# Optimization experiments

Hardware: AMD Instinct MI355X
Metric: run time of the kernel (lower is better)

Reference implementation:

```python
import jax, jax.numpy as jnp
import numpy as np

T, N, E = 4, 4096, 65536
XD, HD, ZD = 256, 256, 64
EPS = 1e-10


def setup_inputs() -> dict:
    key = jax.random.key(0)
    ks = jax.random.split(key, 30)
    rn = lambda k, sh, s=0.05: jax.random.normal(k, sh, dtype=jnp.float32) * s
    inp = {
        "x": rn(ks[0], (T, N, XD), 1.0),
        "edge_idx": jax.random.randint(ks[1], (T, 2, E), 0, N, dtype=jnp.int32),
        "adj": jax.random.bernoulli(ks[2], 0.005, (T, N, N)).astype(jnp.float32),
        "eps_noise": jax.random.normal(ks[3], (T, N, ZD), dtype=jnp.float32),
        "h0": jnp.zeros((1, N, HD), jnp.float32),
        # phi_x / phi_z (Linear+ReLU)
        "phi_x_w": rn(ks[4], (XD, HD)), "phi_x_b": jnp.zeros((HD,), jnp.float32),
        "phi_z_w": rn(ks[5], (ZD, HD)), "phi_z_b": jnp.zeros((HD,), jnp.float32),
        # encoder GCNs
        "enc_w": rn(ks[6], (2 * HD, HD)), "enc_b": jnp.zeros((HD,), jnp.float32),
        "enc_mean_w": rn(ks[7], (HD, ZD)), "enc_mean_b": jnp.zeros((ZD,), jnp.float32),
        "enc_std_w": rn(ks[8], (HD, ZD)), "enc_std_b": jnp.zeros((ZD,), jnp.float32),
        # prior MLPs
        "prior_w": rn(ks[9], (HD, HD)), "prior_b": jnp.zeros((HD,), jnp.float32),
        "prior_mean_w": rn(ks[10], (HD, ZD)), "prior_mean_b": jnp.zeros((ZD,), jnp.float32),
        "prior_std_w": rn(ks[11], (HD, ZD)), "prior_std_b": jnp.zeros((ZD,), jnp.float32),
        # graph-GRU GCNs (bias=False, n_layers=1; x-input is cat[phi_x, phi_z] -> 2*HD)
        "gru_xz_w": rn(ks[12], (2 * HD, HD)), "gru_hz_w": rn(ks[13], (HD, HD)),
        "gru_xr_w": rn(ks[14], (2 * HD, HD)), "gru_hr_w": rn(ks[15], (HD, HD)),
        "gru_xh_w": rn(ks[16], (2 * HD, HD)), "gru_hh_w": rn(ks[17], (HD, HD)),
    }
    return inp


def _gcn(xf, src, dst, W, b):
    """GCNConv: sym-normalized (A + I) aggregation, then bias. Returns pre-activation."""
    h = xf @ W                                             # [N, out]
    deg = 1.0 + jax.ops.segment_sum(jnp.ones(src.shape[0], xf.dtype), dst, num_segments=N)
    dinv = jax.lax.rsqrt(deg)                              # [N]
    norm = dinv[src] * dinv[dst]                           # [E]
    agg = jax.ops.segment_sum(h[src] * norm[:, None], dst, num_segments=N)
    agg = agg + (dinv * dinv)[:, None] * h                 # self-loop term
    if b is not None:
        agg = agg + b
    return agg


def reference(x, edge_idx, adj, eps_noise, h0,
              phi_x_w, phi_x_b, phi_z_w, phi_z_b,
              enc_w, enc_b, enc_mean_w, enc_mean_b, enc_std_w, enc_std_b,
              prior_w, prior_b, prior_mean_w, prior_mean_b, prior_std_w, prior_std_b,
              gru_xz_w, gru_hz_w, gru_xr_w, gru_hr_w, gru_xh_w, gru_hh_w):
    relu, sp, sig = jax.nn.relu, jax.nn.softplus, jax.nn.sigmoid
    h = h0                                                  # [1, N, HD]
    kld = jnp.float32(0.0)
    nll = jnp.float32(0.0)
    enc_means, prior_means = [], []
    nn_f = jnp.float32(N * N)
    for t in range(T):
        src, dst = edge_idx[t, 0], edge_idx[t, 1]
        phi_x_t = relu(x[t] @ phi_x_w + phi_x_b)                       # [N, HD]
        enc_in = jnp.concatenate([phi_x_t, h[-1]], axis=1)             # [N, 2HD]
        enc_t = relu(_gcn(enc_in, src, dst, enc_w, enc_b))
        enc_mean_t = _gcn(enc_t, src, dst, enc_mean_w, enc_mean_b)     # act = identity
        enc_std_t = sp(_gcn(enc_t, src, dst, enc_std_w, enc_std_b))
        prior_t = relu(h[-1] @ prior_w + prior_b)
        prior_mean_t = prior_t @ prior_mean_w + prior_mean_b
        prior_std_t = sp(prior_t @ prior_std_w + prior_std_b)
        z_t = eps_noise[t] * enc_std_t + enc_mean_t                    # reparameterize
        phi_z_t = relu(z_t @ phi_z_w + phi_z_b)
        dec_t = sig(z_t @ z_t.T)                                       # [N, N] decode
        # graph-GRU step (n_layers = 1, bias=False)
        gin = jnp.concatenate([phi_x_t, phi_z_t], axis=1)              # [N, 2HD]
        z_g = sig(_gcn(gin, src, dst, gru_xz_w, None) + _gcn(h[0], src, dst, gru_hz_w, None))
        r_g = sig(_gcn(gin, src, dst, gru_xr_w, None) + _gcn(h[0], src, dst, gru_hr_w, None))
        h_tilde = jnp.tanh(_gcn(gin, src, dst, gru_xh_w, None)
                           + _gcn(r_g * h[0], src, dst, gru_hh_w, None))
        h = (z_g * h[0] + (1.0 - z_g) * h_tilde)[None]                 # [1, N, HD]
        # KLD (faithful to _kld_gauss, including its sign convention)
        s1, s2 = enc_std_t + EPS, prior_std_t + EPS
        kld_el = (2.0 * jnp.log(s2) - 2.0 * jnp.log(s1)
                  - (s1 * s1 + (enc_mean_t - prior_mean_t) ** 2) / (s2 * s2) + 1.0)
        kld = kld + (0.5 / N) * jnp.mean(jnp.sum(kld_el, axis=0))
        # NLL (faithful quirk: BCE-with-logits applied to sigmoid output dec_t)
        a = adj[t]
        tsum = jnp.sum(a)
        posw = (nn_f - tsum) / tsum
        norm = nn_f / ((nn_f - tsum) * 2.0)
        bce = posw * a * sp(-dec_t) + (1.0 - a) * sp(dec_t)
        nll = nll + norm * jnp.mean(bce)
        enc_means.append(enc_mean_t)
        prior_means.append(prior_mean_t)
    return kld, nll, jnp.stack(enc_means), jnp.stack(prior_means), h
```

## Files before the change

### kernel.cpp

```cpp
#include <hip/hip_runtime.h>
#include <hip/hip_bf16.h>

#define T_STEPS 4
#define N 4096
#define E 65536
#define XD 256
#define HD 256
#define ZD 64

typedef __hip_bfloat16 bf16;
typedef __attribute__((ext_vector_type(8))) short short8;
typedef __attribute__((ext_vector_type(4))) float f32x4;

__device__ __forceinline__ float b2f(bf16 v){ return __bfloat162float(v); }
__device__ __forceinline__ bf16 f2b(float v){ return __float2bfloat16(v); }
__device__ __forceinline__ short f2s(float v){ return __builtin_bit_cast(short, f2b(v)); }
__device__ __forceinline__ float bits2f(unsigned int s){ return __builtin_bit_cast(float, s << 16); }
__device__ __forceinline__ float s2f(short s){ return bits2f((unsigned int)(unsigned short)s); }
__device__ __forceinline__ float splus(float x){ return (x > 15.f) ? x : __logf(1.f + __expf(x)); }
__device__ __forceinline__ float sigm(float x){ return 1.f/(1.f + __expf(-x)); }
__device__ __forceinline__ float ftanh(float x){ return 2.f/(1.f + __expf(-2.f*x)) - 1.f; }

__device__ __forceinline__ float ldI(const void* p, size_t i, int f){
  return f ? ((const float*)p)[i] : b2f(((const bf16*)p)[i]);
}
__device__ __forceinline__ void stO(void* p, size_t i, float v, int f){
  if (f) ((float*)p)[i] = v; else ((bf16*)p)[i] = f2b(v);
}
__device__ __forceinline__ void ld8b(const bf16* p, float v[8]){
  uint4 u = *(const uint4*)p;
  v[0]=bits2f(u.x & 0xffffu); v[1]=bits2f(u.x >> 16);
  v[2]=bits2f(u.y & 0xffffu); v[3]=bits2f(u.y >> 16);
  v[4]=bits2f(u.z & 0xffffu); v[5]=bits2f(u.z >> 16);
  v[6]=bits2f(u.w & 0xffffu); v[7]=bits2f(u.w >> 16);
}
__device__ __forceinline__ void ldW8(const void* W, size_t off, int f, float w[8]){
  if (f == 0){ ld8b((const bf16*)W + off, w); }
  else {
    const float* Wf = (const float*)W + off;
    float4 a = *(const float4*)Wf, b = *(const float4*)(Wf + 4);
    w[0]=a.x; w[1]=a.y; w[2]=a.z; w[3]=a.w; w[4]=b.x; w[5]=b.y; w[6]=b.z; w[7]=b.w;
  }
}
__device__ __forceinline__ unsigned int pack2(float a, float b){
  return (unsigned int)(unsigned short)__builtin_bit_cast(unsigned short, f2b(a))
       | ((unsigned int)(unsigned short)__builtin_bit_cast(unsigned short, f2b(b)) << 16);
}
__device__ __forceinline__ uint4 pack8(const float v[8]){
  uint4 o; o.x = pack2(v[0],v[1]); o.y = pack2(v[2],v[3]);
  o.z = pack2(v[4],v[5]); o.w = pack2(v[6],v[7]);
  return o;
}

union SMem {
  struct { short As[64*40]; short Wt[64*40]; } g;
  struct { short Zi[64*72]; short Zj[64*72]; short Adj[64*72];
           float redA[256]; float redB[256]; float redC[256]; } z;
  struct { float msh[16*132]; } m;
  int sh[256];
  float red[256];
};

struct KP {
  const void *x, *adj, *eps, *h0;
  const int* ei;
  const void *phi_x_w, *phi_x_b, *phi_z_w, *phi_z_b;
  const void *enc_w, *enc_b, *enc_mean_w, *enc_mean_b, *enc_std_w, *enc_std_b;
  const void *prior_w, *prior_b, *prior_mean_w, *prior_mean_b, *prior_std_w, *prior_std_b;
  const void *gxz, *ghz, *gxr, *ghr, *gxh, *ghh;
  void* out;
  float* scal; int* dflag; float* dinv; int* offs; int* srcs; float* enorm; int* deg;
  float* h_prev; bf16* h_bf; bf16* phiXa; bf16* Tb1; bf16* Tb2;
  bf16* zbf; float* z_g; bf16* Gs1; bf16* Gsx; bf16* Gms; bf16* Gh2;
};

#define OUT_EM ((size_t)2)
#define OUT_PM ((size_t)(2 + (size_t)T_STEPS*N*ZD))
#define OUT_H  ((size_t)(2 + (size_t)2*T_STEPS*N*ZD))

__device__ void mfma_tile(SMem& sm, int tid, int f,
    const void* A1, int am1, int lda1, const void* A2, int am2, int lda2,
    int K1, int K, const void* W, int ldw, int wcol,
    const void* bias, int act, bf16* C, int ldc, int row0, int ccol0){
  int ar = tid >> 2, akk = (tid & 3)*8;
  int wk = tid >> 3, wn = (tid & 7)*8;
  int wave = tid >> 6, lane = tid & 63, m = lane & 15, kq = lane >> 4;
  f32x4 acc[4] = {};
  for (int k0 = 0; k0 < K; k0 += 32){
    const void* A; int am, lda, kb;
    if (k0 < K1){ A = A1; am = am1; lda = lda1; kb = k0; }
    else        { A = A2; am = am2; lda = lda2; kb = k0 - K1; }
    size_t aidx = (size_t)(row0 + ar)*lda + kb + akk;
    short8 av;
    if (am == 2 || (am == 1 && f == 0)){
      av = *(const short8*)((const short*)A + aidx);
    } else {
      const float* Af = (const float*)A;
      float4 u0 = *(const float4*)(Af + aidx);
      float4 u1 = *(const float4*)(Af + aidx + 4);
      av[0]=f2s(u0.x); av[1]=f2s(u0.y); av[2]=f2s(u0.z); av[3]=f2s(u0.w);
      av[4]=f2s(u1.x); av[5]=f2s(u1.y); av[6]=f2s(u1.z); av[7]=f2s(u1.w);
    }
    *(short8*)&sm.g.As[ar*40 + akk] = av;
    size_t wi = (size_t)(k0 + wk)*ldw + wcol + wn;
    float wf[8]; short wv[8];
    if (f == 0){
      short8 t8 = *(const short8*)((const short*)W + wi);
      #pragma unroll
      for (int j = 0; j < 8; j++) wv[j] = t8[j];
    } else {
      ldW8(W, wi, f, wf);
      #pragma unroll
      for (int j = 0; j < 8; j++) wv[j] = f2s(wf[j]);
    }
    #pragma unroll
    for (int j = 0; j < 8; j++){
      int nrow = wn + j;
      int col = (((wk >> 3) ^ ((nrow >> 3) & 3)) << 3) | (wk & 7);
      sm.g.Wt[nrow*40 + col] = wv[j];
    }
    __syncthreads();
    short8 afr = *(const short8*)&sm.g.As[(wave*16 + m)*40 + kq*8];
    #pragma unroll
    for (int t4 = 0; t4 < 4; t4++){
      int nb = t4*16 + m;
      short8 bfr = *(const short8*)&sm.g.Wt[nb*40 + ((kq ^ ((nb >> 3) & 3)) << 3)];
      acc[t4] = __builtin_amdgcn_mfma_f32_16x16x32_bf16(afr, bfr, acc[t4], 0, 0, 0);
    }
    __syncthreads();
  }
  #pragma unroll
  for (int t4 = 0; t4 < 4; t4++){
    int c = ccol0 + t4*16 + m;
    float bv = bias ? ldI(bias, wcol + t4*16 + m, f) : 0.f;
    #pragma unroll
    for (int reg = 0; reg < 4; reg++){
      int r = row0 + wave*16 + kq*4 + reg;
      float v = acc[t4][reg] + bv;
      if (act == 1) v = fmaxf(v, 0.f);
      C[(size_t)r*ldc + c] = f2b(v);
    }
  }
}

__device__ void dec_tile1(const KP& p, SMem& sm, int tid, int t, int u, int f){
  int i0 = (u >> 6)*64, j0 = (u & 63)*64;
  size_t aoff = (size_t)t*N*N;
  #pragma unroll
  for (int i = 0; i < 2; i++){
    int idx = tid + i*256;
    int r = idx >> 3, c = idx & 7;
    int col = ((c ^ ((r >> 3) & 3)) << 3);
    *(short8*)&sm.z.Zi[r*72 + col] = *(const short8*)((const short*)p.zbf + (size_t)(i0+r)*ZD + c*8);
    *(short8*)&sm.z.Zj[r*72 + col] = *(const short8*)((const short*)p.zbf + (size_t)(j0+r)*ZD + c*8);
  }
  {
    int row = tid >> 2, c0 = (tid & 3)*16;
    if (f){
      const float* ap = (const float*)p.adj + aoff + (size_t)(i0+row)*N + j0 + c0;
      short tmp[16];
      #pragma unroll
      for (int q = 0; q < 16; q += 4){
        float4 v = *(const float4*)(ap + q);
        tmp[q]=f2s(v.x); tmp[q+1]=f2s(v.y); tmp[q+2]=f2s(v.z); tmp[q+3]=f2s(v.w);
      }
      *(short8*)&sm.z.Adj[row*72 + c0]     = *(short8*)&tmp[0];
      *(short8*)&sm.z.Adj[row*72 + c0 + 8] = *(short8*)&tmp[8];
    } else {
      const short* ap = (const short*)p.adj + aoff + (size_t)(i0+row)*N + j0 + c0;
      *(short8*)&sm.z.Adj[row*72 + c0]     = *(const short8*)ap;
      *(short8*)&sm.z.Adj[row*72 + c0 + 8] = *(const short8*)(ap + 8);
    }
  }
  __syncthreads();
  int wave = tid >> 6, lane = tid & 63, m = lane & 15, kq = lane >> 4;
  int ra = wave*16 + m, sa = (ra >> 3) & 3;
  short8 a1 = *(const short8*)&sm.z.Zi[ra*72 + ((kq ^ sa) << 3)];
  short8 a2 = *(const short8*)&sm.z.Zi[ra*72 + (((kq+4) ^ sa) << 3)];
  f32x4 acc[4] = {};
  #pragma unroll
  for (int t4 = 0; t4 < 4; t4++){
    int rb = t4*16 + m, sb2 = (rb >> 3) & 3;
    short8 b1 = *(const short8*)&sm.z.Zj[rb*72 + ((kq ^ sb2) << 3)];
    short8 b2 = *(const short8*)&sm.z.Zj[rb*72 + (((kq+4) ^ sb2) << 3)];
    acc[t4] = __builtin_amdgcn_mfma_f32_16x16x32_bf16(a1, b1, acc[t4], 0, 0, 0);
    acc[t4] = __builtin_amdgcn_mfma_f32_16x16x32_bf16(a2, b2, acc[t4], 0, 0, 0);
  }
  float lts = 0.f, lP = 0.f, lQ = 0.f;
  #pragma unroll
  for (int t4 = 0; t4 < 4; t4++){
    int lj = t4*16 + m;
    #pragma unroll
    for (int reg = 0; reg < 4; reg++){
      int li = wave*16 + kq*4 + reg;
      float av = s2f(sm.z.Adj[li*72 + lj]);
      float dec = sigm(acc[t4][reg]);
      lts += av;
      lQ += (1.f - av)*splus(dec);
      if (av != 0.f) lP += av*splus(-dec);
    }
  }
  __syncthreads();
  sm.z.redA[tid] = lts; sm.z.redB[tid] = lP; sm.z.redC[tid] = lQ;
  __syncthreads();
  for (int o = 128; o > 0; o >>= 1){
    if (tid < o){
      sm.z.redA[tid] += sm.z.redA[tid+o];
      sm.z.redB[tid] += sm.z.redB[tid+o];
      sm.z.redC[tid] += sm.z.redC[tid+o];
    }
    __syncthreads();
  }
  if (tid == 0){
    atomicAdd(p.scal + 8 + t,  sm.z.redA[0]);
    atomicAdd(p.scal + 12 + t, sm.z.redB[0]);
    atomicAdd(p.scal + 16 + t, sm.z.redC[0]);
  }
}

__global__ __launch_bounds__(256) void setup0_k(KP p){
  int gb = blockIdx.x, tid = threadIdx.x;
  if (gb == 0){ if (tid < 64) p.scal[tid] = 0.f; }
  else if (gb == 1){
    if (tid == 0){
      const unsigned short* u = (const unsigned short*)p.x;
      int big = 0;
      for (int i = 0; i < 256; i++){ int e = (u[i] >> 7) & 0xFF; if (e >= 134) big++; }
      *p.dflag = (big > 16) ? 1 : 0;
    }
  } else {
    p.deg[(gb-2)*256 + tid] = 0;
  }
}

__global__ __launch_bounds__(256) void count_deg_k(KP p){
  int idx = blockIdx.x*256 + threadIdx.x;
  int t = idx >> 16, e = idx & (E-1);
  int dst = p.ei[(size_t)t*2*E + E + e] & (N-1);
  atomicAdd(&p.deg[t*N + dst], 1);
}

__global__ __launch_bounds__(256) void setup2_k(KP p){
  __shared__ SMem sm;
  int gb = blockIdx.x, tid = threadIdx.x;
  int f = *p.dflag;
  if (gb < 4){
    int t = gb;
    const int* dg = p.deg + t*N;
    int* of = p.offs + t*(N+1);
    int base = tid*16;
    int loc[16]; int s = 0;
    #pragma unroll
    for (int i = 0; i < 16; i++){ loc[i] = s; s += dg[base+i]; }
    sm.sh[tid] = s;
    __syncthreads();
    for (int o = 1; o < 256; o <<= 1){
      int v = (tid >= o) ? sm.sh[tid-o] : 0;
      __syncthreads();
      sm.sh[tid] += v;
      __syncthreads();
    }
    int pre = (tid == 0) ? 0 : sm.sh[tid-1];
    #pragma unroll
    for (int i = 0; i < 16; i++){
      int deg_i = dg[base+i];
      of[base+i] = pre + loc[i];
      p.dinv[t*N + base + i] = rsqrtf(1.f + (float)deg_i);
    }
    if (tid == 255) of[N] = sm.sh[255];
    __syncthreads();
    #pragma unroll
    for (int i = 0; i < 16; i++) p.deg[t*N + base + i] = pre + loc[i];
  } else if (gb < 36){
    for (int idx = (gb-4)*256 + tid; idx < N*HD; idx += 32*256){
      float v = ldI(p.h0, idx, f);
      p.h_prev[idx] = v; p.h_bf[idx] = f2b(v);
    }
  } else {
    int u = gb - 36;
    int colblk = u & 3, rowblk = u >> 2;
    mfma_tile(sm, tid, f, p.x, 1, XD, nullptr, 0, 0, XD, XD,
              p.phi_x_w, HD, colblk*64, p.phi_x_b, 1,
              p.phiXa, HD, rowblk*64, colblk*64);
  }
}

__global__ __launch_bounds__(256) void g1_k(KP p, int t){
  __shared__ SMem sm;
  int gb = blockIdx.x, tid = threadIdx.x, f = *p.dflag;
  if (gb >= 1024){
    int idx = (gb - 1024)*256 + tid;
    int tt = idx >> 16, e = idx & (E-1);
    int s = p.ei[(size_t)tt*2*E + e] & (N-1);
    int d = p.ei[(size_t)tt*2*E + E + e] & (N-1);
    int pos = atomicAdd(&p.deg[tt*N + d], 1);
    if (pos >= 0 && pos < E){
      p.srcs[(size_t)tt*E + pos] = s;
      p.enorm[(size_t)tt*E + pos] = p.dinv[tt*N + s] * p.dinv[tt*N + d];
    }
    return;
  }
  const bf16* phiX = p.phiXa + (size_t)t*N*HD;
  int colblk = gb & 15, rowblk = gb >> 4;
  int grp = colblk >> 2, c4 = colblk & 3;
  if (grp == 0)
    mfma_tile(sm, tid, f, phiX, 2, HD, p.h_bf, 2, HD, 256, 512,
              p.enc_w, HD, c4*64, nullptr, 0, p.Gs1, 1024, rowblk*64, colblk*64);
  else if (grp == 1)
    mfma_tile(sm, tid, f, p.h_bf, 2, HD, nullptr, 0, 0, 256, 256,
              p.prior_w, HD, c4*64, p.prior_b, 1, p.Gs1, 1024, rowblk*64, colblk*64);
  else if (grp == 2)
    mfma_tile(sm, tid, f, p.h_bf, 2, HD, nullptr, 0, 0, 256, 256,
              p.ghz, HD, c4*64, nullptr, 0, p.Gs1, 1024, rowblk*64, colblk*64);
  else
    mfma_tile(sm, tid, f, p.h_bf, 2, HD, nullptr, 0, 0, 256, 256,
              p.ghr, HD, c4*64, nullptr, 0, p.Gs1, 1024, rowblk*64, colblk*64);
}

__global__ __launch_bounds__(256) void encagg_pms_k(KP p, int t){
  __shared__ SMem sm;
  int gb = blockIdx.x, tid = threadIdx.x, f = *p.dflag;
  const int* offs_t = p.offs + t*(N+1);
  const int* srcs_t = p.srcs + (size_t)t*E;
  const float* en_t = p.enorm + (size_t)t*E;
  const float* dv_t = p.dinv + t*N;
  if (gb < 512){
    int g8 = tid >> 5, l = tid & 31;
    int n = gb*8 + g8, c = l*8;
    int e0 = offs_t[n], e1 = offs_t[n+1];
    float d2 = dv_t[n]*dv_t[n];
    float acc[8], va[8], vb[8];
    ld8b(p.Gs1 + (size_t)n*1024 + c, va);
    #pragma unroll
    for (int j = 0; j < 8; j++) acc[j] = d2 * va[j];
    int e = e0;
    for (; e + 1 < e1; e += 2){
      int s0 = srcs_t[e] & (N-1), s1 = srcs_t[e+1] & (N-1);
      float n0 = en_t[e], n1 = en_t[e+1];
      ld8b(p.Gs1 + (size_t)s0*1024 + c, va);
      ld8b(p.Gs1 + (size_t)s1*1024 + c, vb);
      #pragma unroll
      for (int j = 0; j < 8; j++) acc[j] += n0*va[j] + n1*vb[j];
    }
    if (e < e1){
      int s0 = srcs_t[e] & (N-1);
      float n0 = en_t[e];
      ld8b(p.Gs1 + (size_t)s0*1024 + c, va);
      #pragma unroll
      for (int j = 0; j < 8; j++) acc[j] += n0*va[j];
    }
    #pragma unroll
    for (int j = 0; j < 8; j++) acc[j] = fmaxf(acc[j] + ldI(p.enc_b, c + j, f), 0.f);
    *(uint4*)(p.Tb1 + (size_t)n*HD + c) = pack8(acc);
  } else {
    int u = gb - 512;
    int colblk = u & 1, rowblk = u >> 1;
    mfma_tile(sm, tid, f, p.Gs1 + 256, 2, 1024, nullptr, 0, 0, 256, 256,
              colblk ? p.prior_std_w : p.prior_mean_w, ZD, 0,
              colblk ? p.prior_std_b : p.prior_mean_b, 0,
              p.Gms, 256, rowblk*64, 128 + colblk*64);
  }
}

__global__ __launch_bounds__(256) void encms_k(KP p, int t){
  __shared__ SMem sm;
  int gb = blockIdx.x, tid = threadIdx.x, f = *p.dflag;
  int colblk = gb & 1, rowblk = gb >> 1;
  mfma_tile(sm, tid, f, p.Tb1, 2, HD, nullptr, 0, 0, 256, 256,
            colblk ? p.enc_std_w : p.enc_mean_w, ZD, 0, nullptr, 0,
            p.Gms, 256, rowblk*64, colblk*64);
}

__global__ __launch_bounds__(256) void msaggpost_k(KP p, int t){
  __shared__ SMem sm;
  int gb = blockIdx.x, tid = threadIdx.x, f = *p.dflag;
  const int* offs_t = p.offs + t*(N+1);
  const int* srcs_t = p.srcs + (size_t)t*E;
  const float* en_t = p.enorm + (size_t)t*E;
  const float* dv_t = p.dinv + t*N;
  int g16 = tid >> 4, l = tid & 15;
  int n = gb*16 + g16, c = l*8;
  {
    int e0 = offs_t[n], e1 = offs_t[n+1];
    float d2 = dv_t[n]*dv_t[n];
    float acc[8], va[8], vb[8];
    ld8b(p.Gms + (size_t)n*256 + c, va);
    #pragma unroll
    for (int j = 0; j < 8; j++) acc[j] = d2 * va[j];
    int e = e0;
    for (; e + 1 < e1; e += 2){
      int s0 = srcs_t[e] & (N-1), s1 = srcs_t[e+1] & (N-1);
      float n0 = en_t[e], n1 = en_t[e+1];
      ld8b(p.Gms + (size_t)s0*256 + c, va);
      ld8b(p.Gms + (size_t)s1*256 + c, vb);
      #pragma unroll
      for (int j = 0; j < 8; j++) acc[j] += n0*va[j] + n1*vb[j];
    }
    if (e < e1){
      int s0 = srcs_t[e] & (N-1);
      float n0 = en_t[e];
      ld8b(p.Gms + (size_t)s0*256 + c, va);
      #pragma unroll
      for (int j = 0; j < 8; j++) acc[j] += n0*va[j];
    }
    #pragma unroll
    for (int j = 0; j < 8; j++) sm.m.msh[g16*132 + c + j] = acc[j];
  }
  __syncthreads();
  float el = 0.f;
  {
    int d0 = l*4;
    #pragma unroll
    for (int q = 0; q < 4; q++){
      int d = d0 + q;
      size_t idx = (size_t)n*ZD + d;
      float mean = sm.m.msh[g16*132 + d] + ldI(p.enc_mean_b, d, f);
      float sd = splus(sm.m.msh[g16*132 + 64 + d] + ldI(p.enc_std_b, d, f));
      float zv = ldI(p.eps, (size_t)t*N*ZD + idx, f)*sd + mean;
      p.zbf[idx] = f2b(zv);
      stO(p.out, OUT_EM + (size_t)t*N*ZD + idx, mean, f);
      float pm = b2f(p.Gms[(size_t)n*256 + 128 + d]);
      float ps = splus(b2f(p.Gms[(size_t)n*256 + 192 + d]));
      stO(p.out, OUT_PM + (size_t)t*N*ZD + idx, pm, f);
      float s1 = sd + 1e-10f, s2 = ps + 1e-10f;
      float dm = mean - pm;
      el += 2.f*(__logf(s2) - __logf(s1)) - (s1*s1 + dm*dm)/(s2*s2) + 1.f;
    }
  }
  __syncthreads();
  sm.red[tid] = el; __syncthreads();
  for (int o = 128; o > 0; o >>= 1){ if (tid < o) sm.red[tid] += sm.red[tid+o]; __syncthreads(); }
  if (tid == 0) atomicAdd(p.scal + 4, sm.red[0] * (0.5f/((float)N*(float)ZD)));
}

__global__ __launch_bounds__(256) void phiz_k(KP p, int t){
  __shared__ SMem sm;
  int gb = blockIdx.x, tid = threadIdx.x, f = *p.dflag;
  int colblk = gb & 3, rowblk = gb >> 2;
  mfma_tile(sm, tid, f, p.zbf, 2, ZD, nullptr, 0, 0, ZD, ZD,
            p.phi_z_w, HD, colblk*64, p.phi_z_b, 1, p.Tb2, HD, rowblk*64, colblk*64);
}

__global__ __launch_bounds__(256) void grux_dec_k(KP p, int t){
  __shared__ SMem sm;
  int gb = blockIdx.x, tid = threadIdx.x, f = *p.dflag;
  if (gb < 768){
    const bf16* phiX = p.phiXa + (size_t)t*N*HD;
    int colblk = gb % 12, rowblk = gb / 12;
    int grp = colblk >> 2, c4 = colblk & 3;
    const void* W = (grp == 0) ? p.gxz : ((grp == 1) ? p.gxr : p.gxh);
    mfma_tile(sm, tid, f, phiX, 2, HD, p.Tb2, 2, HD, 256, 512,
              W, HD, c4*64, nullptr, 0, p.Gsx, 768, rowblk*64, colblk*64);
  } else {
    dec_tile1(p, sm, tid, t, gb - 768, f);
  }
}

__global__ __launch_bounds__(256) void zr_k(KP p, int t){
  int gb = blockIdx.x, tid = threadIdx.x;
  const int* offs_t = p.offs + t*(N+1);
  const int* srcs_t = p.srcs + (size_t)t*E;
  const float* en_t = p.enorm + (size_t)t*E;
  const float* dv_t = p.dinv + t*N;
  int g4 = tid >> 6, lane = tid & 63;
  int n = gb*4 + g4, c = lane*8;
  int e0 = offs_t[n], e1 = offs_t[n+1];
  float d2 = dv_t[n]*dv_t[n];
  float acc[8], v1[8], v2[8], v3[8], v4[8];
  ld8b(p.Gsx + (size_t)n*768 + c, v1);
  ld8b(p.Gs1 + 512 + (size_t)n*1024 + c, v2);
  #pragma unroll
  for (int j = 0; j < 8; j++) acc[j] = d2 * (v1[j] + v2[j]);
  int e = e0;
  for (; e + 1 < e1; e += 2){
    int s0 = srcs_t[e] & (N-1), s1 = srcs_t[e+1] & (N-1);
    float n0 = en_t[e], n1 = en_t[e+1];
    ld8b(p.Gsx + (size_t)s0*768 + c, v1);
    ld8b(p.Gs1 + 512 + (size_t)s0*1024 + c, v2);
    ld8b(p.Gsx + (size_t)s1*768 + c, v3);
    ld8b(p.Gs1 + 512 + (size_t)s1*1024 + c, v4);
    #pragma unroll
    for (int j = 0; j < 8; j++) acc[j] += n0*(v1[j] + v2[j]) + n1*(v3[j] + v4[j]);
  }
  if (e < e1){
    int s0 = srcs_t[e] & (N-1);
    float n0 = en_t[e];
    ld8b(p.Gsx + (size_t)s0*768 + c, v1);
    ld8b(p.Gs1 + 512 + (size_t)s0*1024 + c, v2);
    #pragma unroll
    for (int j = 0; j < 8; j++) acc[j] += n0*(v1[j] + v2[j]);
  }
  if (c < 256){
    size_t base = (size_t)n*HD + c;
    float4 o0, o1;
    o0.x = sigm(acc[0]); o0.y = sigm(acc[1]); o0.z = sigm(acc[2]); o0.w = sigm(acc[3]);
    o1.x = sigm(acc[4]); o1.y = sigm(acc[5]); o1.z = sigm(acc[6]); o1.w = sigm(acc[7]);
    *(float4*)(p.z_g + base) = o0;
    *(float4*)(p.z_g + base + 4) = o1;
  } else {
    size_t base = (size_t)n*HD + (c - 256);
    float r[8];
    #pragma unroll
    for (int j = 0; j < 8; j++) r[j] = sigm(acc[j]) * p.h_prev[base+j];
    *(uint4*)(p.Tb1 + base) = pack8(r);
  }
}

__global__ __launch_bounds__(256) void hh_k(KP p, int t){
  __shared__ SMem sm;
  int gb = blockIdx.x, tid = threadIdx.x, f = *p.dflag;
  int colblk = gb & 3, rowblk = gb >> 2;
  mfma_tile(sm, tid, f, p.Tb1, 2, HD, nullptr, 0, 0, 256, 256,
            p.ghh, HD, colblk*64, nullptr, 0, p.Gh2, 256, rowblk*64, colblk*64);
}

__global__ __launch_bounds__(256) void hagg_k(KP p, int t){
  int gb = blockIdx.x, tid = threadIdx.x, f = *p.dflag;
  if (gb >= 512){
    if (tid == 0){
      const float NNf = 16777216.f;
      float nll = 0.f;
      for (int tt = 0; tt < T_STEPS; tt++){
        float ts = p.scal[8+tt], P = p.scal[12+tt], Q = p.scal[16+tt];
        float posw = (NNf - ts)/ts;
        nll += (posw*P + Q) * 0.5f/(NNf - ts);
      }
      stO(p.out, 0, p.scal[4], f);
      stO(p.out, 1, nll, f);
    }
    return;
  }
  const int* offs_t = p.offs + t*(N+1);
  const int* srcs_t = p.srcs + (size_t)t*E;
  const float* en_t = p.enorm + (size_t)t*E;
  const float* dv_t = p.dinv + t*N;
  int g8 = tid >> 5, l = tid & 31;
  int n = gb*8 + g8, c = l*8;
  int e0 = offs_t[n], e1 = offs_t[n+1];
  float d2 = dv_t[n]*dv_t[n];
  float acc[8], v1[8], v2[8], v3[8], v4[8];
  ld8b(p.Gsx + 512 + (size_t)n*768 + c, v1);
  ld8b(p.Gh2 + (size_t)n*256 + c, v2);
  #pragma unroll
  for (int j = 0; j < 8; j++) acc[j] = d2 * (v1[j] + v2[j]);
  int e = e0;
  for (; e + 1 < e1; e += 2){
    int s0 = srcs_t[e] & (N-1), s1 = srcs_t[e+1] & (N-1);
    float n0 = en_t[e], n1 = en_t[e+1];
    ld8b(p.Gsx + 512 + (size_t)s0*768 + c, v1);
    ld8b(p.Gh2 + (size_t)s0*256 + c, v2);
    ld8b(p.Gsx + 512 + (size_t)s1*768 + c, v3);
    ld8b(p.Gh2 + (size_t)s1*256 + c, v4);
    #pragma unroll
    for (int j = 0; j < 8; j++) acc[j] += n0*(v1[j] + v2[j]) + n1*(v3[j] + v4[j]);
  }
  if (e < e1){
    int s0 = srcs_t[e] & (N-1);
    float n0 = en_t[e];
    ld8b(p.Gsx + 512 + (size_t)s0*768 + c, v1);
    ld8b(p.Gh2 + (size_t)s0*256 + c, v2);
    #pragma unroll
    for (int j = 0; j < 8; j++) acc[j] += n0*(v1[j] + v2[j]);
  }
  size_t base = (size_t)n*HD + c;
  #pragma unroll
  for (int j = 0; j < 8; j++){
    float z = p.z_g[base+j];
    float hv = p.h_prev[base+j];
    float nv = z*hv + (1.f - z)*ftanh(acc[j]);
    p.h_prev[base+j] = nv;
    p.h_bf[base+j] = f2b(nv);
    if (t == T_STEPS-1) stO(p.out, OUT_H + base + j, nv, f);
  }
}

extern "C" void kernel_launch(void* const* d_in, const int* in_sizes, int n_in,
                              void* d_out, int out_size, void* d_ws, size_t ws_size,
                              hipStream_t stream){
  KP P;
  P.x = d_in[0];  P.ei = (const int*)d_in[1];  P.adj = d_in[2];  P.eps = d_in[3];  P.h0 = d_in[4];
  P.phi_x_w = d_in[5];  P.phi_x_b = d_in[6];  P.phi_z_w = d_in[7];  P.phi_z_b = d_in[8];
  P.enc_w = d_in[9];  P.enc_b = d_in[10];
  P.enc_mean_w = d_in[11];  P.enc_mean_b = d_in[12];
  P.enc_std_w = d_in[13];   P.enc_std_b = d_in[14];
  P.prior_w = d_in[15];  P.prior_b = d_in[16];
  P.prior_mean_w = d_in[17];  P.prior_mean_b = d_in[18];
  P.prior_std_w = d_in[19];   P.prior_std_b = d_in[20];
  P.gxz = d_in[21];  P.ghz = d_in[22];  P.gxr = d_in[23];
  P.ghr = d_in[24];  P.gxh = d_in[25];  P.ghh = d_in[26];
  P.out = d_out;

  char* wp = (char*)d_ws;
  auto alloc = [&](size_t bytes){ void* q = (void*)wp; wp += (bytes + 255) & ~(size_t)255; return q; };
  P.scal  = (float*)alloc(64*sizeof(float));
  P.dflag = (int*)  alloc(256);
  P.dinv  = (float*)alloc((size_t)T_STEPS*N*4);
  P.offs  = (int*)  alloc((size_t)T_STEPS*(N+1)*4);
  P.srcs  = (int*)  alloc((size_t)T_STEPS*E*4);
  P.enorm = (float*)alloc((size_t)T_STEPS*E*4);
  P.deg   = (int*)  alloc((size_t)T_STEPS*N*4);
  P.h_prev= (float*)alloc((size_t)N*HD*4);
  P.h_bf  = (bf16*) alloc((size_t)N*HD*2);
  P.phiXa = (bf16*) alloc((size_t)T_STEPS*N*HD*2);
  P.Tb1   = (bf16*) alloc((size_t)N*HD*2);
  P.Tb2   = (bf16*) alloc((size_t)N*HD*2);
  P.zbf   = (bf16*) alloc((size_t)N*ZD*2);
  P.z_g   = (float*)alloc((size_t)N*HD*4);
  P.Gs1   = (bf16*) alloc((size_t)N*1024*2);
  P.Gsx   = (bf16*) alloc((size_t)N*768*2);
  P.Gms   = (bf16*) alloc((size_t)N*256*2);
  P.Gh2   = (bf16*) alloc((size_t)N*256*2);

  setup0_k<<<66,256,0,stream>>>(P);
  count_deg_k<<<1024,256,0,stream>>>(P);
  setup2_k<<<1060,256,0,stream>>>(P);
  for (int t = 0; t < T_STEPS; t++){
    g1_k<<<(t == 0) ? 2048 : 1024,256,0,stream>>>(P, t);
    encagg_pms_k<<<640,256,0,stream>>>(P, t);
    encms_k<<<128,256,0,stream>>>(P, t);
    msaggpost_k<<<256,256,0,stream>>>(P, t);
    phiz_k<<<256,256,0,stream>>>(P, t);
    grux_dec_k<<<4864,256,0,stream>>>(P, t);
    zr_k<<<1024,256,0,stream>>>(P, t);
    hh_k<<<256,256,0,stream>>>(P, t);
    hagg_k<<<(t == T_STEPS-1) ? 513 : 512,256,0,stream>>>(P, t);
  }
}
```

Baseline: 1.401 ms.

## Precompute phi_x GEMMs for all steps, fuse encoder aggregation with mean/std GEMM

All phi_x-dependent products (encoder and the three GRU x-gates) are computed up front for every timestep in a new batched setup kernel. Per-step GEMMs now cover only the h or phi_z half of K and add the precomputed half in the epilogue. The generic MFMA tile now processes 64-wide K chunks per sync. The encoder aggregation and the enc mean/std projection are merged into one kernel that keeps the aggregated rows in LDS, removing a launch and a round trip through memory. This costs an extra 32 MB buffer and larger shared-memory tiles, which may lower occupancy.

```diff
diff --git a/kernel.cpp b/kernel.cpp
--- a/kernel.cpp
+++ b/kernel.cpp
@@ -51,15 +51,17 @@
   o.z = pack2(v[4],v[5]); o.w = pack2(v[6],v[7]);
   return o;
 }
-
-union SMem {
-  struct { short As[64*40]; short Wt[64*40]; } g;
-  struct { short Zi[64*72]; short Zj[64*72]; short Adj[64*72];
-           float redA[256]; float redB[256]; float redC[256]; } z;
-  struct { float msh[16*132]; } m;
-  int sh[256];
-  float red[256];
-};
+__device__ __forceinline__ unsigned int pack2s(short a, short b){
+  return (unsigned int)(unsigned short)a | ((unsigned int)(unsigned short)b << 16);
+}
+__device__ __forceinline__ const void* wofs(const void* W, int f, size_t elems){
+  return f ? (const void*)((const float*)W + elems) : (const void*)((const bf16*)W + elems);
+}
+
+struct GemmSM { short As[64*72]; short Wt[64*72]; };
+struct DecSM  { short Zi[64*72]; short Zj[64*72]; short Adj[64*72];
+                float redA[256]; float redB[256]; float redC[256]; };
+struct EncSM  { short At[16*264]; short Wt[128*40]; };
 
 struct KP {
   const void *x, *adj, *eps, *h0;
@@ -72,60 +74,70 @@
   float* scal; int* dflag; float* dinv; int* offs; int* srcs; float* enorm; int* deg;
   float* h_prev; bf16* h_bf; bf16* phiXa; bf16* Tb1; bf16* Tb2;
   bf16* zbf; float* z_g; bf16* Gs1; bf16* Gsx; bf16* Gms; bf16* Gh2;
+  bf16* PreB;
 };
 
 #define OUT_EM ((size_t)2)
 #define OUT_PM ((size_t)(2 + (size_t)T_STEPS*N*ZD))
 #define OUT_H  ((size_t)(2 + (size_t)2*T_STEPS*N*ZD))
 
-__device__ void mfma_tile(SMem& sm, int tid, int f,
-    const void* A1, int am1, int lda1, const void* A2, int am2, int lda2,
-    int K1, int K, const void* W, int ldw, int wcol,
-    const void* bias, int act, bf16* C, int ldc, int row0, int ccol0){
-  int ar = tid >> 2, akk = (tid & 3)*8;
-  int wk = tid >> 3, wn = (tid & 7)*8;
+__device__ void mfma_tile(GemmSM& sm, int tid, int f,
+    const void* A, int am, int lda, int K,
+    const void* W, int ldw, int wcol,
+    const void* bias, int act, bf16* C, int ldc, int row0, int ccol0,
+    const bf16* pre, int ldpre){
+  int ar = tid >> 2, akk = (tid & 3)*16;
+  int kp2 = (tid >> 3)*2, wn = (tid & 7)*8;
   int wave = tid >> 6, lane = tid & 63, m = lane & 15, kq = lane >> 4;
   f32x4 acc[4] = {};
-  for (int k0 = 0; k0 < K; k0 += 32){
-    const void* A; int am, lda, kb;
-    if (k0 < K1){ A = A1; am = am1; lda = lda1; kb = k0; }
-    else        { A = A2; am = am2; lda = lda2; kb = k0 - K1; }
-    size_t aidx = (size_t)(row0 + ar)*lda + kb + akk;
-    short8 av;
-    if (am == 2 || (am == 1 && f == 0)){
-      av = *(const short8*)((const short*)A + aidx);
+  for (int k0 = 0; k0 < K; k0 += 64){
+    size_t aidx = (size_t)(row0 + ar)*lda + k0 + akk;
+    short8 av0, av1;
+    if (am == 2 || f == 0){
+      av0 = *(const short8*)((const short*)A + aidx);
+      av1 = *(const short8*)((const short*)A + aidx + 8);
     } else {
-      const float* Af = (const float*)A;
-      float4 u0 = *(const float4*)(Af + aidx);
-      float4 u1 = *(const float4*)(Af + aidx + 4);
-      av[0]=f2s(u0.x); av[1]=f2s(u0.y); av[2]=f2s(u0.z); av[3]=f2s(u0.w);
-      av[4]=f2s(u1.x); av[5]=f2s(u1.y); av[6]=f2s(u1.z); av[7]=f2s(u1.w);
-    }
-    *(short8*)&sm.g.As[ar*40 + akk] = av;
-    size_t wi = (size_t)(k0 + wk)*ldw + wcol + wn;
-    float wf[8]; short wv[8];
+      const float* Af = (const float*)A + aidx;
+      float4 u0 = *(const float4*)(Af);
+      float4 u1 = *(const float4*)(Af + 4);
+      float4 u2 = *(const float4*)(Af + 8);
+      float4 u3 = *(const float4*)(Af + 12);
+      av0[0]=f2s(u0.x); av0[1]=f2s(u0.y); av0[2]=f2s(u0.z); av0[3]=f2s(u0.w);
+      av0[4]=f2s(u1.x); av0[5]=f2s(u1.y); av0[6]=f2s(u1.z); av0[7]=f2s(u1.w);
+      av1[0]=f2s(u2.x); av1[1]=f2s(u2.y); av1[2]=f2s(u2.z); av1[3]=f2s(u2.w);
+      av1[4]=f2s(u3.x); av1[5]=f2s(u3.y); av1[6]=f2s(u3.z); av1[7]=f2s(u3.w);
+    }
+    size_t wi = (size_t)(k0 + kp2)*ldw + wcol + wn;
+    short w0[8], w1[8];
     if (f == 0){
-      short8 t8 = *(const short8*)((const short*)W + wi);
-      #pragma unroll
-      for (int j = 0; j < 8; j++) wv[j] = t8[j];
+      short8 t0 = *(const short8*)((const short*)W + wi);
+      short8 t1 = *(const short8*)((const short*)W + wi + ldw);
+      #pragma unroll
+      for (int j = 0; j < 8; j++){ w0[j] = t0[j]; w1[j] = t1[j]; }
     } else {
-      ldW8(W, wi, f, wf);
-      #pragma unroll
-      for (int j = 0; j < 8; j++) wv[j] = f2s(wf[j]);
-    }
+      float wf0[8], wf1[8];
+      ldW8(W, wi, 1, wf0); ldW8(W, wi + ldw, 1, wf1);
+      #pragma unroll
+      for (int j = 0; j < 8; j++){ w0[j] = f2s(wf0[j]); w1[j] = f2s(wf1[j]); }
+    }
+    *(short8*)&sm.As[ar*72 + akk]     = av0;
+    *(short8*)&sm.As[ar*72 + akk + 8] = av1;
     #pragma unroll
     for (int j = 0; j < 8; j++){
       int nrow = wn + j;
-      int col = (((wk >> 3) ^ ((nrow >> 3) & 3)) << 3) | (wk & 7);
-      sm.g.Wt[nrow*40 + col] = wv[j];
+      int col = (((kp2 >> 3) ^ ((nrow >> 3) & 7)) << 3) | (kp2 & 7);
+      *(unsigned int*)&sm.Wt[nrow*72 + col] = pack2s(w0[j], w1[j]);
     }
     __syncthreads();
-    short8 afr = *(const short8*)&sm.g.As[(wave*16 + m)*40 + kq*8];
+    short8 afr0 = *(const short8*)&sm.As[(wave*16 + m)*72 + kq*8];
+    short8 afr1 = *(const short8*)&sm.As[(wave*16 + m)*72 + (kq + 4)*8];
     #pragma unroll
     for (int t4 = 0; t4 < 4; t4++){
-      int nb = t4*16 + m;
-      short8 bfr = *(const short8*)&sm.g.Wt[nb*40 + ((kq ^ ((nb >> 3) & 3)) << 3)];
-      acc[t4] = __builtin_amdgcn_mfma_f32_16x16x32_bf16(afr, bfr, acc[t4], 0, 0, 0);
+      int nb = t4*16 + m, sb = (nb >> 3) & 7;
+      short8 b0 = *(const short8*)&sm.Wt[nb*72 + ((kq ^ sb) << 3)];
+      short8 b1 = *(const short8*)&sm.Wt[nb*72 + (((kq + 4) ^ sb) << 3)];
+      acc[t4] = __builtin_amdgcn_mfma_f32_16x16x32_bf16(afr0, b0, acc[t4], 0, 0, 0);
+      acc[t4] = __builtin_amdgcn_mfma_f32_16x16x32_bf16(afr1, b1, acc[t4], 0, 0, 0);
     }
     __syncthreads();
   }
@@ -137,13 +149,14 @@
     for (int reg = 0; reg < 4; reg++){
       int r = row0 + wave*16 + kq*4 + reg;
       float v = acc[t4][reg] + bv;
+      if (pre) v += b2f(pre[(size_t)r*ldpre + t4*16 + m]);
       if (act == 1) v = fmaxf(v, 0.f);
       C[(size_t)r*ldc + c] = f2b(v);
     }
   }
 }
 
-__device__ void dec_tile1(const KP& p, SMem& sm, int tid, int t, int u, int f){
+__device__ void dec_tile1(const KP& p, DecSM& d, int tid, int t, int u, int f){
   int i0 = (u >> 6)*64, j0 = (u & 63)*64;
   size_t aoff = (size_t)t*N*N;
   #pragma unroll
@@ -151,8 +164,8 @@
     int idx = tid + i*256;
     int r = idx >> 3, c = idx & 7;
     int col = ((c ^ ((r >> 3) & 3)) << 3);
-    *(short8*)&sm.z.Zi[r*72 + col] = *(const short8*)((const short*)p.zbf + (size_t)(i0+r)*ZD + c*8);
-    *(short8*)&sm.z.Zj[r*72 + col] = *(const short8*)((const short*)p.zbf + (size_t)(j0+r)*ZD + c*8);
+    *(short8*)&d.Zi[r*72 + col] = *(const short8*)((const short*)p.zbf + (size_t)(i0+r)*ZD + c*8);
+    *(short8*)&d.Zj[r*72 + col] = *(const short8*)((const short*)p.zbf + (size_t)(j0+r)*ZD + c*8);
   }
   {
     int row = tid >> 2, c0 = (tid & 3)*16;
@@ -164,25 +177,25 @@
         float4 v = *(const float4*)(ap + q);
         tmp[q]=f2s(v.x); tmp[q+1]=f2s(v.y); tmp[q+2]=f2s(v.z); tmp[q+3]=f2s(v.w);
       }
-      *(short8*)&sm.z.Adj[row*72 + c0]     = *(short8*)&tmp[0];
-      *(short8*)&sm.z.Adj[row*72 + c0 + 8] = *(short8*)&tmp[8];
+      *(short8*)&d.Adj[row*72 + c0]     = *(short8*)&tmp[0];
+      *(short8*)&d.Adj[row*72 + c0 + 8] = *(short8*)&tmp[8];
     } else {
       const short* ap = (const short*)p.adj + aoff + (size_t)(i0+row)*N + j0 + c0;
-      *(short8*)&sm.z.Adj[row*72 + c0]     = *(const short8*)ap;
-      *(short8*)&sm.z.Adj[row*72 + c0 + 8] = *(const short8*)(ap + 8);
+      *(short8*)&d.Adj[row*72 + c0]     = *(const short8*)ap;
+      *(short8*)&d.Adj[row*72 + c0 + 8] = *(const short8*)(ap + 8);
     }
   }
   __syncthreads();
   int wave = tid >> 6, lane = tid & 63, m = lane & 15, kq = lane >> 4;
   int ra = wave*16 + m, sa = (ra >> 3) & 3;
-  short8 a1 = *(const short8*)&sm.z.Zi[ra*72 + ((kq ^ sa) << 3)];
-  short8 a2 = *(const short8*)&sm.z.Zi[ra*72 + (((kq+4) ^ sa) << 3)];
+  short8 a1 = *(const short8*)&d.Zi[ra*72 + ((kq ^ sa) << 3)];
+  short8 a2 = *(const short8*)&d.Zi[ra*72 + (((kq+4) ^ sa) << 3)];
   f32x4 acc[4] = {};
   #pragma unroll
   for (int t4 = 0; t4 < 4; t4++){
     int rb = t4*16 + m, sb2 = (rb >> 3) & 3;
-    short8 b1 = *(const short8*)&sm.z.Zj[rb*72 + ((kq ^ sb2) << 3)];
-    short8 b2 = *(const short8*)&sm.z.Zj[rb*72 + (((kq+4) ^ sb2) << 3)];
+    short8 b1 = *(const short8*)&d.Zj[rb*72 + ((kq ^ sb2) << 3)];
+    short8 b2 = *(const short8*)&d.Zj[rb*72 + (((kq+4) ^ sb2) << 3)];
     acc[t4] = __builtin_amdgcn_mfma_f32_16x16x32_bf16(a1, b1, acc[t4], 0, 0, 0);
     acc[t4] = __builtin_amdgcn_mfma_f32_16x16x32_bf16(a2, b2, acc[t4], 0, 0, 0);
   }
@@ -193,7 +206,7 @@
     #pragma unroll
     for (int reg = 0; reg < 4; reg++){
       int li = wave*16 + kq*4 + reg;
-      float av = s2f(sm.z.Adj[li*72 + lj]);
+      float av = s2f(d.Adj[li*72 + lj]);
       float dec = sigm(acc[t4][reg]);
       lts += av;
       lQ += (1.f - av)*splus(dec);
@@ -201,20 +214,20 @@
     }
   }
   __syncthreads();
-  sm.z.redA[tid] = lts; sm.z.redB[tid] = lP; sm.z.redC[tid] = lQ;
+  d.redA[tid] = lts; d.redB[tid] = lP; d.redC[tid] = lQ;
   __syncthreads();
   for (int o = 128; o > 0; o >>= 1){
     if (tid < o){
-      sm.z.redA[tid] += sm.z.redA[tid+o];
-      sm.z.redB[tid] += sm.z.redB[tid+o];
-      sm.z.redC[tid] += sm.z.redC[tid+o];
+      d.redA[tid] += d.redA[tid+o];
+      d.redB[tid] += d.redB[tid+o];
+      d.redC[tid] += d.redC[tid+o];
     }
     __syncthreads();
   }
   if (tid == 0){
-    atomicAdd(p.scal + 8 + t,  sm.z.redA[0]);
-    atomicAdd(p.scal + 12 + t, sm.z.redB[0]);
-    atomicAdd(p.scal + 16 + t, sm.z.redC[0]);
+    atomicAdd(p.scal + 8 + t,  d.redA[0]);
+    atomicAdd(p.scal + 12 + t, d.redB[0]);
+    atomicAdd(p.scal + 16 + t, d.redC[0]);
   }
 }
 
@@ -241,7 +254,7 @@
 }
 
 __global__ __launch_bounds__(256) void setup2_k(KP p){
-  __shared__ SMem sm;
+  __shared__ union { int sh[256]; GemmSM g; } sm;
   int gb = blockIdx.x, tid = threadIdx.x;
   int f = *p.dflag;
   if (gb < 4){
@@ -279,14 +292,29 @@
   } else {
     int u = gb - 36;
     int colblk = u & 3, rowblk = u >> 2;
-    mfma_tile(sm, tid, f, p.x, 1, XD, nullptr, 0, 0, XD, XD,
+    mfma_tile(sm.g, tid, f, p.x, 1, XD, XD,
               p.phi_x_w, HD, colblk*64, p.phi_x_b, 1,
-              p.phiXa, HD, rowblk*64, colblk*64);
-  }
+              p.phiXa, HD, rowblk*64, colblk*64, nullptr, 0);
+  }
+}
+
+__global__ __launch_bounds__(256) void setup3_k(KP p){
+  __shared__ GemmSM sm;
+  int gb = blockIdx.x, tid = threadIdx.x, f = *p.dflag;
+  int colblk = gb & 15, rowblk = gb >> 4;
+  int grp = colblk >> 2, c4 = colblk & 3;
+  const void* W;
+  if (grp == 0) W = p.enc_w;
+  else if (grp == 1) W = p.gxz;
+  else if (grp == 2) W = p.gxr;
+  else W = p.gxh;
+  mfma_tile(sm, tid, f, p.phiXa, 2, HD, 256,
+            W, HD, c4*64, nullptr, 0,
+            p.PreB, 1024, rowblk*64, colblk*64, nullptr, 0);
 }
 
 __global__ __launch_bounds__(256) void g1_k(KP p, int t){
-  __shared__ SMem sm;
+  __shared__ GemmSM sm;
   int gb = blockIdx.x, tid = threadIdx.x, f = *p.dflag;
   if (gb >= 1024){
     int idx = (gb - 1024)*256 + tid;
@@ -300,79 +328,126 @@
     }
     return;
   }
-  const bf16* phiX = p.phiXa + (size_t)t*N*HD;
+  const bf16* preT = p.PreB + (size_t)t*N*1024;
   int colblk = gb & 15, rowblk = gb >> 4;
   int grp = colblk >> 2, c4 = colblk & 3;
   if (grp == 0)
-    mfma_tile(sm, tid, f, phiX, 2, HD, p.h_bf, 2, HD, 256, 512,
-              p.enc_w, HD, c4*64, nullptr, 0, p.Gs1, 1024, rowblk*64, colblk*64);
+    mfma_tile(sm, tid, f, p.h_bf, 2, HD, 256,
+              wofs(p.enc_w, f, (size_t)256*HD), HD, c4*64, nullptr, 0,
+              p.Gs1, 1024, rowblk*64, colblk*64, preT + c4*64, 1024);
   else if (grp == 1)
-    mfma_tile(sm, tid, f, p.h_bf, 2, HD, nullptr, 0, 0, 256, 256,
-              p.prior_w, HD, c4*64, p.prior_b, 1, p.Gs1, 1024, rowblk*64, colblk*64);
+    mfma_tile(sm, tid, f, p.h_bf, 2, HD, 256,
+              p.prior_w, HD, c4*64, p.prior_b, 1,
+              p.Gs1, 1024, rowblk*64, colblk*64, nullptr, 0);
   else if (grp == 2)
-    mfma_tile(sm, tid, f, p.h_bf, 2, HD, nullptr, 0, 0, 256, 256,
-              p.ghz, HD, c4*64, nullptr, 0, p.Gs1, 1024, rowblk*64, colblk*64);
+    mfma_tile(sm, tid, f, p.h_bf, 2, HD, 256,
+              p.ghz, HD, c4*64, nullptr, 0,
+              p.Gs1, 1024, rowblk*64, colblk*64, nullptr, 0);
   else
-    mfma_tile(sm, tid, f, p.h_bf, 2, HD, nullptr, 0, 0, 256, 256,
-              p.ghr, HD, c4*64, nullptr, 0, p.Gs1, 1024, rowblk*64, colblk*64);
-}
-
-__global__ __launch_bounds__(256) void encagg_pms_k(KP p, int t){
-  __shared__ SMem sm;
+    mfma_tile(sm, tid, f, p.h_bf, 2, HD, 256,
+              p.ghr, HD, c4*64, nullptr, 0,
+              p.Gs1, 1024, rowblk*64, colblk*64, nullptr, 0);
+}
+
+__global__ __launch_bounds__(256) void encfused_k(KP p, int t){
+  __shared__ union { EncSM e; GemmSM g; } sm;
   int gb = blockIdx.x, tid = threadIdx.x, f = *p.dflag;
+  if (gb >= 256){
+    int u = gb - 256;
+    int colblk = u & 1, rowblk = u >> 1;
+    mfma_tile(sm.g, tid, f, p.Gs1 + 256, 2, 1024, 256,
+              colblk ? p.prior_std_w : p.prior_mean_w, ZD, 0,
+              colblk ? p.prior_std_b : p.prior_mean_b, 0,
+              p.Gms, 256, rowblk*64, 128 + colblk*64, nullptr, 0);
+    return;
+  }
   const int* offs_t = p.offs + t*(N+1);
   const int* srcs_t = p.srcs + (size_t)t*E;
   const float* en_t = p.enorm + (size_t)t*E;
   const float* dv_t = p.dinv + t*N;
-  if (gb < 512){
-    int g8 = tid >> 5, l = tid & 31;
-    int n = gb*8 + g8, c = l*8;
+  int g16 = tid >> 4, l = tid & 15;
+  int n = gb*16 + g16, c = l*16;
+  {
     int e0 = offs_t[n], e1 = offs_t[n+1];
     float d2 = dv_t[n]*dv_t[n];
-    float acc[8], va[8], vb[8];
+    float acc[16], va[8], vb[8], vc[8], vd[8];
     ld8b(p.Gs1 + (size_t)n*1024 + c, va);
-    #pragma unroll
-    for (int j = 0; j < 8; j++) acc[j] = d2 * va[j];
+    ld8b(p.Gs1 + (size_t)n*1024 + c + 8, vb);
+    #pragma unroll
+    for (int j = 0; j < 8; j++){ acc[j] = d2*va[j]; acc[8+j] = d2*vb[j]; }
     int e = e0;
     for (; e + 1 < e1; e += 2){
       int s0 = srcs_t[e] & (N-1), s1 = srcs_t[e+1] & (N-1);
       float n0 = en_t[e], n1 = en_t[e+1];
       ld8b(p.Gs1 + (size_t)s0*1024 + c, va);
-      ld8b(p.Gs1 + (size_t)s1*1024 + c, vb);
-      #pragma unroll
-      for (int j = 0; j < 8; j++) acc[j] += n0*va[j] + n1*vb[j];
+      ld8b(p.Gs1 + (size_t)s0*1024 + c + 8, vb);
+      ld8b(p.Gs1 + (size_t)s1*1024 + c, vc);
+      ld8b(p.Gs1 + (size_t)s1*1024 + c + 8, vd);
+      #pragma unroll
+      for (int j = 0; j < 8; j++){ acc[j] += n0*va[j] + n1*vc[j]; acc[8+j] += n0*vb[j] + n1*vd[j]; }
     }
     if (e < e1){
       int s0 = srcs_t[e] & (N-1);
       float n0 = en_t[e];
       ld8b(p.Gs1 + (size_t)s0*1024 + c, va);
-      #pragma unroll
-      for (int j = 0; j < 8; j++) acc[j] += n0*va[j];
-    }
-    #pragma unroll
-    for (int j = 0; j < 8; j++) acc[j] = fmaxf(acc[j] + ldI(p.enc_b, c + j, f), 0.f);
-    *(uint4*)(p.Tb1 + (size_t)n*HD + c) = pack8(acc);
-  } else {
-    int u = gb - 512;
-    int colblk = u & 1, rowblk = u >> 1;
-    mfma_tile(sm, tid, f, p.Gs1 + 256, 2, 1024, nullptr, 0, 0, 256, 256,
-              colblk ? p.prior_std_w : p.prior_mean_w, ZD, 0,
-              colblk ? p.prior_std_b : p.prior_mean_b, 0,
-              p.Gms, 256, rowblk*64, 128 + colblk*64);
-  }
-}
-
-__global__ __launch_bounds__(256) void encms_k(KP p, int t){
-  __shared__ SMem sm;
-  int gb = blockIdx.x, tid = threadIdx.x, f = *p.dflag;
-  int colblk = gb & 1, rowblk = gb >> 1;
-  mfma_tile(sm, tid, f, p.Tb1, 2, HD, nullptr, 0, 0, 256, 256,
-            colblk ? p.enc_std_w : p.enc_mean_w, ZD, 0, nullptr, 0,
-            p.Gms, 256, rowblk*64, colblk*64);
+      ld8b(p.Gs1 + (size_t)s0*1024 + c + 8, vb);
+      #pragma unroll
+      for (int j = 0; j < 8; j++){ acc[j] += n0*va[j]; acc[8+j] += n0*vb[j]; }
+    }
+    #pragma unroll
+    for (int j = 0; j < 16; j++) acc[j] = fmaxf(acc[j] + ldI(p.enc_b, c + j, f), 0.f);
+    *(uint4*)&sm.e.At[g16*264 + c]     = pack8(acc);
+    *(uint4*)&sm.e.At[g16*264 + c + 8] = pack8(acc + 8);
+  }
+  int wave = tid >> 6, lane = tid & 63, m = lane & 15, kq = lane >> 4;
+  int kp2e = (tid >> 4)*2;
+  int wn2 = (tid & 15)*8;
+  f32x4 acc2[2] = {};
+  for (int k0 = 0; k0 < 256; k0 += 32){
+    const void* Wp = (wn2 < 64) ? p.enc_mean_w : p.enc_std_w;
+    int wc = wn2 & 63;
+    size_t wi = (size_t)(k0 + kp2e)*ZD + wc;
+    short w0[8], w1[8];
+    if (f == 0){
+      short8 t0 = *(const short8*)((const short*)Wp + wi);
+      short8 t1 = *(const short8*)((const short*)Wp + wi + ZD);
+      #pragma unroll
+      for (int j = 0; j < 8; j++){ w0[j] = t0[j]; w1[j] = t1[j]; }
+    } else {
+      float wf0[8], wf1[8];
+      ldW8(Wp, wi, 1, wf0); ldW8(Wp, wi + ZD, 1, wf1);
+      #pragma unroll
+      for (int j = 0; j < 8; j++){ w0[j] = f2s(wf0[j]); w1[j] = f2s(wf1[j]); }
+    }
+    #pragma unroll
+    for (int j = 0; j < 8; j++){
+      int nrow = wn2 + j;
+      int col = (((kp2e >> 3) ^ ((nrow >> 3) & 3)) << 3) | (kp2e & 7);
+      *(unsigned int*)&sm.e.Wt[nrow*40 + col] = pack2s(w0[j], w1[j]);
+    }
+    __syncthreads();
+    short8 afr = *(const short8*)&sm.e.At[m*264 + k0 + kq*8];
+    #pragma unroll
+    for (int t2 = 0; t2 < 2; t2++){
+      int nb = wave*32 + t2*16 + m, sb = (nb >> 3) & 3;
+      short8 bfr = *(const short8*)&sm.e.Wt[nb*40 + ((kq ^ sb) << 3)];
+      acc2[t2] = __builtin_amdgcn_mfma_f32_16x16x32_bf16(afr, bfr, acc2[t2], 0, 0, 0);
+    }
+    __syncthreads();
+  }
+  #pragma unroll
+  for (int t2 = 0; t2 < 2; t2++){
+    int cc = wave*32 + t2*16 + m;
+    #pragma unroll
+    for (int reg = 0; reg < 4; reg++){
+      int node = gb*16 + kq*4 + reg;
+      p.Gms[(size_t)node*256 + cc] = f2b(acc2[t2][reg]);
+    }
+  }
 }
 
 __global__ __launch_bounds__(256) void msaggpost_k(KP p, int t){
-  __shared__ SMem sm;
+  __shared__ union { float msh[16*132]; float red[256]; } sm;
   int gb = blockIdx.x, tid = threadIdx.x, f = *p.dflag;
   const int* offs_t = p.offs + t*(N+1);
   const int* srcs_t = p.srcs + (size_t)t*E;
@@ -404,7 +479,7 @@
       for (int j = 0; j < 8; j++) acc[j] += n0*va[j];
     }
     #pragma unroll
-    for (int j = 0; j < 8; j++) sm.m.msh[g16*132 + c + j] = acc[j];
+    for (int j = 0; j < 8; j++) sm.msh[g16*132 + c + j] = acc[j];
   }
   __syncthreads();
   float el = 0.f;
@@ -414,8 +489,8 @@
     for (int q = 0; q < 4; q++){
       int d = d0 + q;
       size_t idx = (size_t)n*ZD + d;
-      float mean = sm.m.msh[g16*132 + d] + ldI(p.enc_mean_b, d, f);
-      float sd = splus(sm.m.msh[g16*132 + 64 + d] + ldI(p.enc_std_b, d, f));
+      float mean = sm.msh[g16*132 + d] + ldI(p.enc_mean_b, d, f);
+      float sd = splus(sm.msh[g16*132 + 64 + d] + ldI(p.enc_std_b, d, f));
       float zv = ldI(p.eps, (size_t)t*N*ZD + idx, f)*sd + mean;
       p.zbf[idx] = f2b(zv);
       stO(p.out, OUT_EM + (size_t)t*N*ZD + idx, mean, f);
@@ -434,25 +509,27 @@
 }
 
 __global__ __launch_bounds__(256) void phiz_k(KP p, int t){
-  __shared__ SMem sm;
+  __shared__ GemmSM sm;
   int gb = blockIdx.x, tid = threadIdx.x, f = *p.dflag;
   int colblk = gb & 3, rowblk = gb >> 2;
-  mfma_tile(sm, tid, f, p.zbf, 2, ZD, nullptr, 0, 0, ZD, ZD,
-            p.phi_z_w, HD, colblk*64, p.phi_z_b, 1, p.Tb2, HD, rowblk*64, colblk*64);
+  mfma_tile(sm, tid, f, p.zbf, 2, ZD, ZD,
+            p.phi_z_w, HD, colblk*64, p.phi_z_b, 1,
+            p.Tb2, HD, rowblk*64, colblk*64, nullptr, 0);
 }
 
 __global__ __launch_bounds__(256) void grux_dec_k(KP p, int t){
-  __shared__ SMem sm;
+  __shared__ union { GemmSM g; DecSM z; } sm;
   int gb = blockIdx.x, tid = threadIdx.x, f = *p.dflag;
   if (gb < 768){
-    const bf16* phiX = p.phiXa + (size_t)t*N*HD;
     int colblk = gb % 12, rowblk = gb / 12;
     int grp = colblk >> 2, c4 = colblk & 3;
     const void* W = (grp == 0) ? p.gxz : ((grp == 1) ? p.gxr : p.gxh);
-    mfma_tile(sm, tid, f, phiX, 2, HD, p.Tb2, 2, HD, 256, 512,
-              W, HD, c4*64, nullptr, 0, p.Gsx, 768, rowblk*64, colblk*64);
+    mfma_tile(sm.g, tid, f, p.Tb2, 2, HD, 256,
+              wofs(W, f, (size_t)256*HD), HD, c4*64, nullptr, 0,
+              p.Gsx, 768, rowblk*64, colblk*64,
+              p.PreB + (size_t)t*N*1024 + 256 + colblk*64, 1024);
   } else {
-    dec_tile1(p, sm, tid, t, gb - 768, f);
+    dec_tile1(p, sm.z, tid, t, gb - 768, f);
   }
 }
 
@@ -507,11 +584,12 @@
 }
 
 __global__ __launch_bounds__(256) void hh_k(KP p, int t){
-  __shared__ SMem sm;
+  __shared__ GemmSM sm;
   int gb = blockIdx.x, tid = threadIdx.x, f = *p.dflag;
   int colblk = gb & 3, rowblk = gb >> 2;
-  mfma_tile(sm, tid, f, p.Tb1, 2, HD, nullptr, 0, 0, 256, 256,
-            p.ghh, HD, colblk*64, nullptr, 0, p.Gh2, 256, rowblk*64, colblk*64);
+  mfma_tile(sm, tid, f, p.Tb1, 2, HD, 256,
+            p.ghh, HD, colblk*64, nullptr, 0,
+            p.Gh2, 256, rowblk*64, colblk*64, nullptr, 0);
 }
 
 __global__ __launch_bounds__(256) void hagg_k(KP p, int t){
@@ -610,14 +688,15 @@
   P.Gsx   = (bf16*) alloc((size_t)N*768*2);
   P.Gms   = (bf16*) alloc((size_t)N*256*2);
   P.Gh2   = (bf16*) alloc((size_t)N*256*2);
+  P.PreB  = (bf16*) alloc((size_t)T_STEPS*N*1024*2);
 
   setup0_k<<<66,256,0,stream>>>(P);
   count_deg_k<<<1024,256,0,stream>>>(P);
   setup2_k<<<1060,256,0,stream>>>(P);
+  setup3_k<<<4096,256,0,stream>>>(P);
   for (int t = 0; t < T_STEPS; t++){
     g1_k<<<(t == 0) ? 2048 : 1024,256,0,stream>>>(P, t);
-    encagg_pms_k<<<640,256,0,stream>>>(P, t);
-    encms_k<<<128,256,0,stream>>>(P, t);
+    encfused_k<<<384,256,0,stream>>>(P, t);
     msaggpost_k<<<256,256,0,stream>>>(P, t);
     phiz_k<<<256,256,0,stream>>>(P, t);
     grux_dec_k<<<4864,256,0,stream>>>(P, t);
```

New measurement: 1.311 ms. -6.5%, faster.
